# Performance work log

Hardware: AMD Instinct MI355X
Metric: run time of the kernel (lower is better)

## Reference

```python
import jax, jax.numpy as jnp
import numpy as np

MODEL = 1024
HEADS = 16
HEAD_DIM = MODEL // HEADS
INNER = 4096
EPS = 1e-5


def _layer_norm(x, gamma, beta):
    mu = jnp.mean(x, axis=-1, keepdims=True)
    var = jnp.mean((x - mu) ** 2, axis=-1, keepdims=True)
    return (x - mu) * jax.lax.rsqrt(var + EPS) * gamma + beta


def setup_inputs() -> dict:
    key = jax.random.key(0)
    ks = jax.random.split(key, 12)
    B, S = 4, 2048
    s_in = 1.0 / np.sqrt(MODEL)
    s_ff = 1.0 / np.sqrt(INNER)
    return {
        "x": jax.random.normal(ks[0], (B, S, MODEL), jnp.float32),
        "mask": jnp.ones((B, 1, 1, S), jnp.int32),
        "Wq": jax.random.normal(ks[1], (MODEL, MODEL), jnp.float32) * s_in,
        "bq": jnp.zeros((MODEL,), jnp.float32),
        "Wk": jax.random.normal(ks[2], (MODEL, MODEL), jnp.float32) * s_in,
        "bk": jnp.zeros((MODEL,), jnp.float32),
        "Wv": jax.random.normal(ks[3], (MODEL, MODEL), jnp.float32) * s_in,
        "bv": jnp.zeros((MODEL,), jnp.float32),
        "Wo": jax.random.normal(ks[4], (MODEL, MODEL), jnp.float32) * s_in,
        "bo": jnp.zeros((MODEL,), jnp.float32),
        "g1": jnp.ones((MODEL,), jnp.float32),
        "beta1": jnp.zeros((MODEL,), jnp.float32),
        "W1": jax.random.normal(ks[5], (MODEL, INNER), jnp.float32) * s_in,
        "b1": jnp.zeros((INNER,), jnp.float32),
        "W2": jax.random.normal(ks[6], (INNER, MODEL), jnp.float32) * s_ff,
        "b2": jnp.zeros((MODEL,), jnp.float32),
        "g2": jnp.ones((MODEL,), jnp.float32),
        "beta2": jnp.zeros((MODEL,), jnp.float32),
    }


def reference(x, mask, Wq, bq, Wk, bk, Wv, bv, Wo, bo, g1, beta1, W1, b1, W2, b2, g2, beta2):
    B, S, _ = x.shape
    temp = jnp.sqrt(jnp.float32(HEAD_DIM))
    # projections -> [B, H, S, Dh]
    q = (x @ Wq + bq).reshape(B, S, HEADS, HEAD_DIM).transpose(0, 2, 1, 3)
    k = (x @ Wk + bk).reshape(B, S, HEADS, HEAD_DIM).transpose(0, 2, 1, 3)
    v = (x @ Wv + bv).reshape(B, S, HEADS, HEAD_DIM).transpose(0, 2, 1, 3)
    # scores [B, H, S, S]
    scores = jnp.einsum("bhqd,bhkd->bhqk", q / temp, k)
    scores = jnp.where(mask == 0, jnp.float32(-1e10), scores)
    attn = jax.nn.softmax(scores, axis=-1)
    ctx = jnp.einsum("bhqk,bhkd->bhqd", attn, v)
    ctx = ctx.transpose(0, 2, 1, 3).reshape(B, S, MODEL)
    attn_out = ctx @ Wo + bo
    x = _layer_norm(x + attn_out, g1, beta1)
    ff = jax.nn.relu(x @ W1 + b1) @ W2 + b2
    x = _layer_norm(x + ff, g2, beta2)
    return x
```

## Files before the change

### kernel.cpp

```cpp
#include <hip/hip_runtime.h>
#include <stdint.h>

#define MODEL 1024
#define INNER 4096
#define NHEADS 16
#define HDIM 64
#define BATCH 4
#define SEQ 2048
#define MROWS (BATCH*SEQ)

#define QSCALE 0.18033688011112042f
#define DEFER_THR 11.541560327111708f

typedef __bf16 bf16x8 __attribute__((ext_vector_type(8)));
typedef float f32x4 __attribute__((ext_vector_type(4)));
typedef unsigned short ushort4v __attribute__((ext_vector_type(4)));

extern "C" __device__ float __ocml_native_exp2_f32(float);

__device__ __forceinline__ unsigned short f2bf(float f) {
  unsigned u = __builtin_bit_cast(unsigned, f);
  u += 0x7FFFu + ((u >> 16) & 1u);
  return (unsigned short)(u >> 16);
}
__device__ __forceinline__ unsigned packbf_trunc(float lo, float hi) {
  return (__builtin_bit_cast(unsigned, hi) & 0xFFFF0000u) |
         (__builtin_bit_cast(unsigned, lo) >> 16);
}

#define AS1 __attribute__((address_space(1)))
#define AS3 __attribute__((address_space(3)))
__device__ __forceinline__ void gload_lds16(const void* g, void* l) {
  __builtin_amdgcn_global_load_lds((const AS1 void*)g, (AS3 void*)l, 16, 0, 0);
}

__global__ __launch_bounds__(256) void k_cvt(const float* __restrict__ in,
                                             unsigned short* __restrict__ out, int n4) {
  int i = blockIdx.x * 256 + threadIdx.x;
  if (i < n4) {
    float4 v = ((const float4*)in)[i];
    ushort4v o = { f2bf(v.x), f2bf(v.y), f2bf(v.z), f2bf(v.w) };
    ((ushort4v*)out)[i] = o;
  }
}

__global__ __launch_bounds__(256) void k_bcat(const float* __restrict__ bq,
                                              const float* __restrict__ bk,
                                              const float* __restrict__ bv,
                                              float* __restrict__ o) {
  int i = blockIdx.x * 256 + threadIdx.x;
  o[i] = (i < 1024) ? bq[i] : (i < 2048) ? bk[i - 1024] : bv[i - 2048];
}

__global__ __launch_bounds__(256) void k_transpose(const float* __restrict__ W,
                                                   unsigned short* __restrict__ Wt,
                                                   int K, int N) {
  __shared__ float tile[32][33];
  const int n0 = blockIdx.x * 32, k0 = blockIdx.y * 32;
  const int c = threadIdx.x & 31, r4 = threadIdx.x >> 5;
#pragma unroll
  for (int i = 0; i < 4; i++) {
    int r = r4 + i * 8;
    tile[r][c] = W[(size_t)(k0 + r) * N + n0 + c];
  }
  __syncthreads();
#pragma unroll
  for (int i = 0; i < 4; i++) {
    int r = r4 + i * 8;
    Wt[(size_t)(n0 + r) * K + k0 + c] = f2bf(tile[c][r]);
  }
}

template <int MODE, bool SPLIT>
__global__ __launch_bounds__(512, 2) void k_gemm(const unsigned short* __restrict__ A,
                                                 const unsigned short* __restrict__ Bt,
                                                 const float* __restrict__ bias,
                                                 void* __restrict__ out0,
                                                 void* __restrict__ out1,
                                                 void* __restrict__ out2,
                                                 int M, int N, int Kfull) {
  __shared__ unsigned short As[3 * 256 * 32];
  __shared__ unsigned short Bs[3 * 256 * 32];
  const int t = threadIdx.x;
  const int lane = t & 63;
  const int w = t >> 6;
  const int li = lane & 15, lg = lane >> 4;
  const int wm8 = w >> 2, wn4 = w & 3;

  const unsigned nwg = gridDim.x * gridDim.y;
  const unsigned lin = blockIdx.y * gridDim.x + blockIdx.x;
  const unsigned q8 = nwg >> 3, r8 = nwg & 7, xcd = lin & 7, pos = lin >> 3;
  const unsigned swz = (xcd < r8 ? xcd * (q8 + 1) : r8 * (q8 + 1) + (xcd - r8) * q8) + pos;
  int bx = swz % gridDim.x, by = swz / gridDim.x;

  int kp = 0, Ksub = Kfull;
  if (SPLIT) {
    const int hx = gridDim.x >> 1;
    kp = bx >= hx;
    bx -= kp * hx;
    Ksub = Kfull >> 1;
  }
  const int bm = by * 256, bn = bx * 256;
  const size_t koff = (size_t)kp * Ksub;
  const int NT = Ksub / 32;

  const int sr0 = w * 16 + (lane >> 2);
  const int sr1 = sr0 + 128;
  const int sl = lane & 3;
  const unsigned short* pA0 = A + (size_t)(bm + sr0) * Kfull + koff + ((sl ^ ((sr0 >> 1) & 3)) << 3);
  const unsigned short* pA1 = A + (size_t)(bm + sr1) * Kfull + koff + ((sl ^ ((sr1 >> 1) & 3)) << 3);
  const unsigned short* pB0 = Bt + (size_t)(bn + sr0) * Kfull + koff + ((sl ^ ((sr0 >> 1) & 3)) << 3);
  const unsigned short* pB1 = Bt + (size_t)(bn + sr1) * Kfull + koff + ((sl ^ ((sr1 >> 1) & 3)) << 3);

  f32x4 acc[8][4] = {};

  auto stageA = [&](int buf, int tt) {
    gload_lds16(pA0 + tt * 32, &As[buf * 8192 + w * 512]);
    gload_lds16(pA1 + tt * 32, &As[buf * 8192 + 4096 + w * 512]);
  };
  auto stageB = [&](int buf, int tt) {
    gload_lds16(pB0 + tt * 32, &Bs[buf * 8192 + w * 512]);
    gload_lds16(pB1 + tt * 32, &Bs[buf * 8192 + 4096 + w * 512]);
  };

  stageA(0, 0); stageB(0, 0);
  stageA(1, 1); stageB(1, 1);
  asm volatile("s_waitcnt vmcnt(4)" ::: "memory");
  __builtin_amdgcn_s_barrier();

  int buf = 0;
  for (int tt = 0; tt < NT; ++tt) {
    const int nb = (buf + 2 >= 3) ? buf - 1 : buf + 2;
    const unsigned short* Ab = &As[buf * 8192];
    const unsigned short* Bb = &Bs[buf * 8192];
    bf16x8 av[4], bv_[4];
#pragma unroll
    for (int m = 0; m < 4; m++) {
      const int r = wm8 * 128 + m * 16 + li;
      av[m] = *(const bf16x8*)&Ab[r * 32 + ((lg ^ ((r >> 1) & 3)) << 3)];
    }
#pragma unroll
    for (int n = 0; n < 4; n++) {
      const int r = wn4 * 64 + n * 16 + li;
      bv_[n] = *(const bf16x8*)&Bb[r * 32 + ((lg ^ ((r >> 1) & 3)) << 3)];
    }
    if (tt + 2 < NT) stageA(nb, tt + 2);
    __builtin_amdgcn_s_barrier();
    __builtin_amdgcn_s_setprio(1);
#pragma unroll
    for (int m = 0; m < 4; m++)
#pragma unroll
      for (int n = 0; n < 4; n++)
        acc[m][n] = __builtin_amdgcn_mfma_f32_16x16x32_bf16(av[m], bv_[n], acc[m][n], 0, 0, 0);
    __builtin_amdgcn_s_setprio(0);
    bf16x8 av2[4];
#pragma unroll
    for (int m = 0; m < 4; m++) {
      const int r = wm8 * 128 + 64 + m * 16 + li;
      av2[m] = *(const bf16x8*)&Ab[r * 32 + ((lg ^ ((r >> 1) & 3)) << 3)];
    }
    if (tt + 2 < NT) stageB(nb, tt + 2);
    __builtin_amdgcn_s_barrier();
    __builtin_amdgcn_s_setprio(1);
#pragma unroll
    for (int m = 0; m < 4; m++)
#pragma unroll
      for (int n = 0; n < 4; n++)
        acc[m + 4][n] = __builtin_amdgcn_mfma_f32_16x16x32_bf16(av2[m], bv_[n], acc[m + 4][n], 0, 0, 0);
    __builtin_amdgcn_s_setprio(0);
    if (tt + 2 < NT) asm volatile("s_waitcnt vmcnt(4)" ::: "memory");
    else             asm volatile("s_waitcnt vmcnt(0)" ::: "memory");
    __builtin_amdgcn_s_barrier();
    buf = (buf == 2) ? 0 : buf + 1;
  }

#pragma unroll
  for (int m = 0; m < 8; m++) {
    const int row0 = bm + wm8 * 128 + m * 16 + lg * 4;
#pragma unroll
    for (int n = 0; n < 4; n++) {
      const int gcol = bn + wn4 * 64 + n * 16 + li;
      if (MODE == 0) {
        float* dst = (float*)(kp ? out1 : out0);
        const float bvc = (!SPLIT || kp == 0) ? bias[gcol] : 0.f;
#pragma unroll
        for (int j = 0; j < 4; j++)
          dst[(size_t)(row0 + j) * N + gcol] = acc[m][n][j] + bvc;
      } else if (MODE == 2) {
        const float bvc = bias[gcol];
#pragma unroll
        for (int j = 0; j < 4; j++)
          ((unsigned short*)out0)[(size_t)(row0 + j) * N + gcol] = f2bf(fmaxf(acc[m][n][j] + bvc, 0.f));
      } else {
        const float bvc = bias[gcol];
        const int region = gcol >> 10, lcol = gcol & 1023;
        if (region < 2) {
          unsigned short* dst = (unsigned short*)(region ? out1 : out0);
          const float sc = region ? 1.f : QSCALE;
#pragma unroll
          for (int j = 0; j < 4; j++)
            dst[(size_t)(row0 + j) * MODEL + lcol] = f2bf((acc[m][n][j] + bvc) * sc);
        } else {
          ushort4v o = {f2bf(acc[m][n][0] + bvc), f2bf(acc[m][n][1] + bvc),
                        f2bf(acc[m][n][2] + bvc), f2bf(acc[m][n][3] + bvc)};
          *(ushort4v*)&((unsigned short*)out2)[(size_t)lcol * MROWS + row0] = o;
        }
      }
    }
  }
}

__global__ __launch_bounds__(256, 3) void k_attn(const unsigned short* __restrict__ q,
                                                 const unsigned short* __restrict__ kptr,
                                                 const unsigned short* __restrict__ vt,
                                                 const int* __restrict__ mask,
                                                 unsigned short* __restrict__ ctx) {
  __shared__ unsigned short Ks[2][64 * 64];
  __shared__ unsigned short Vs[2][64 * 64];
  __shared__ unsigned short Ps[4][32 * 64];
  const int t = threadIdx.x, lane = t & 63, w = t >> 6;
  const int li = lane & 15, lg = lane >> 4;
  const int bh = blockIdx.y, b = bh >> 4, h = bh & 15;
  const int q0 = blockIdx.x * 128;
  const size_t basebs = (size_t)b * SEQ;
  const int sw = 8 * (li & 7);
  const int srow = lane >> 3;
  const int scsw = ((lane & 7) ^ srow) * 8;

  auto stageKV = [&](int buf, int kt) {
#pragma unroll
    for (int i = 0; i < 2; i++) {
      const int row = i * 32 + w * 8 + srow;
      gload_lds16(kptr + (basebs + kt + row) * MODEL + h * 64 + scsw,
                  &Ks[buf][i * 2048 + w * 512]);
    }
#pragma unroll
    for (int i = 0; i < 2; i++) {
      const int row = i * 32 + w * 8 + srow;
      gload_lds16(vt + (size_t)(h * 64 + row) * MROWS + basebs + kt + scsw,
                  &Vs[buf][i * 2048 + w * 512]);
    }
  };

  stageKV(0, 0);

  bf16x8 qf[2][2];
#pragma unroll
  for (int m = 0; m < 2; m++)
#pragma unroll
    for (int kk = 0; kk < 2; kk++) {
      int row = q0 + w * 32 + m * 16 + li;
      qf[m][kk] = *(const bf16x8*)&q[(basebs + row) * MODEL + h * 64 + kk * 32 + lg * 8];
    }

  const unsigned short one_bits = 0x3F80;
  const __bf16 oneb = __builtin_bit_cast(__bf16, one_bits);
  const bf16x8 ones = {oneb, oneb, oneb, oneb, oneb, oneb, oneb, oneb};

  f32x4 acc_oT[4][2] = {};
  f32x4 acc_l[2] = {};
  float mrow[2] = {-3e38f, -3e38f};

  int cur = 0;
  for (int kt = 0; kt < SEQ; kt += 64) {
    int4 mk4[4];
#pragma unroll
    for (int n = 0; n < 4; n++)
      mk4[n] = *(const int4*)&mask[b * SEQ + kt + n * 16 + lg * 4];

    const bool notlast = (kt + 64 < SEQ);
    if (notlast) {
      stageKV(cur ^ 1, kt + 64);
      asm volatile("s_waitcnt vmcnt(8)" ::: "memory");
    } else {
      asm volatile("s_waitcnt vmcnt(4)" ::: "memory");
    }
    __builtin_amdgcn_s_barrier();

    f32x4 sacc[2][4] = {};
    __builtin_amdgcn_s_setprio(1);
#pragma unroll
    for (int n = 0; n < 4; n++) {
      const int rb = (n * 16 + li) * 64;
      bf16x8 kf0 = *(const bf16x8*)&Ks[cur][rb + ((lg * 8) ^ sw)];
      bf16x8 kf1 = *(const bf16x8*)&Ks[cur][rb + ((32 + lg * 8) ^ sw)];
#pragma unroll
      for (int m = 0; m < 2; m++) {
        sacc[m][n] = __builtin_amdgcn_mfma_f32_16x16x32_bf16(kf0, qf[m][0], sacc[m][n], 0, 0, 0);
        sacc[m][n] = __builtin_amdgcn_mfma_f32_16x16x32_bf16(kf1, qf[m][1], sacc[m][n], 0, 0, 0);
      }
    }
    __builtin_amdgcn_s_setprio(0);

    int mand = mk4[0].x & mk4[0].y & mk4[0].z & mk4[0].w;
    mand &= mk4[1].x & mk4[1].y & mk4[1].z & mk4[1].w;
    mand &= mk4[2].x & mk4[2].y & mk4[2].z & mk4[2].w;
    mand &= mk4[3].x & mk4[3].y & mk4[3].z & mk4[3].w;
    const bool fast = __all(mand != 0);

#pragma unroll
    for (int m = 0; m < 2; m++) {
      if (!fast) {
#pragma unroll
        for (int n = 0; n < 4; n++) {
          const int mks[4] = {mk4[n].x, mk4[n].y, mk4[n].z, mk4[n].w};
#pragma unroll
          for (int j = 0; j < 4; j++)
            sacc[m][n][j] = (mks[j] == 0) ? -1e30f : sacc[m][n][j];
        }
      }
      float t0 = fmaxf(fmaxf(sacc[m][0][0], sacc[m][0][1]), fmaxf(sacc[m][0][2], sacc[m][0][3]));
      float t1 = fmaxf(fmaxf(sacc[m][1][0], sacc[m][1][1]), fmaxf(sacc[m][1][2], sacc[m][1][3]));
      float t2 = fmaxf(fmaxf(sacc[m][2][0], sacc[m][2][1]), fmaxf(sacc[m][2][2], sacc[m][2][3]));
      float t3 = fmaxf(fmaxf(sacc[m][3][0], sacc[m][3][1]), fmaxf(sacc[m][3][2], sacc[m][3][3]));
      float rmax = fmaxf(fmaxf(t0, t1), fmaxf(t2, t3));
      rmax = fmaxf(rmax, __shfl_xor(rmax, 16));
      rmax = fmaxf(rmax, __shfl_xor(rmax, 32));
      if (!__all(rmax <= mrow[m] + DEFER_THR)) {
        float mnew = fmaxf(mrow[m], rmax);
        float alpha = __ocml_native_exp2_f32(mrow[m] - mnew);
        mrow[m] = mnew;
        acc_l[m] *= alpha;
#pragma unroll
        for (int nd = 0; nd < 4; nd++)
#pragma unroll
          for (int j = 0; j < 4; j++) acc_oT[nd][m][j] *= alpha;
      }
#pragma unroll
      for (int n = 0; n < 4; n++) {
        float p0 = __ocml_native_exp2_f32(sacc[m][n][0] - mrow[m]);
        float p1 = __ocml_native_exp2_f32(sacc[m][n][1] - mrow[m]);
        float p2 = __ocml_native_exp2_f32(sacc[m][n][2] - mrow[m]);
        float p3 = __ocml_native_exp2_f32(sacc[m][n][3] - mrow[m]);
        uint2 pk = {packbf_trunc(p0, p1), packbf_trunc(p2, p3)};
        *(uint2*)&Ps[w][(m * 16 + li) * 64 + ((n * 16 + lg * 4) ^ sw)] = pk;
      }
    }
    asm volatile("s_waitcnt lgkmcnt(0)" ::: "memory");

    __builtin_amdgcn_s_setprio(1);
#pragma unroll
    for (int n2 = 0; n2 < 2; n2++) {
      const int kof = (n2 * 32 + lg * 8) ^ sw;
      bf16x8 pa0 = *(const bf16x8*)&Ps[w][li * 64 + kof];
      bf16x8 pa1 = *(const bf16x8*)&Ps[w][(16 + li) * 64 + kof];
#pragma unroll
      for (int nd = 0; nd < 4; nd++) {
        bf16x8 vfr = *(const bf16x8*)&Vs[cur][(nd * 16 + li) * 64 + kof];
        acc_oT[nd][0] = __builtin_amdgcn_mfma_f32_16x16x32_bf16(vfr, pa0, acc_oT[nd][0], 0, 0, 0);
        acc_oT[nd][1] = __builtin_amdgcn_mfma_f32_16x16x32_bf16(vfr, pa1, acc_oT[nd][1], 0, 0, 0);
      }
      acc_l[0] = __builtin_amdgcn_mfma_f32_16x16x32_bf16(ones, pa0, acc_l[0], 0, 0, 0);
      acc_l[1] = __builtin_amdgcn_mfma_f32_16x16x32_bf16(ones, pa1, acc_l[1], 0, 0, 0);
    }
    __builtin_amdgcn_s_setprio(0);
    __builtin_amdgcn_sched_barrier(0);
    __builtin_amdgcn_s_barrier();
    cur ^= 1;
  }

#pragma unroll
  for (int m = 0; m < 2; m++) {
    const float rl = 1.f / acc_l[m][0];
    const size_t rowoff = (basebs + q0 + w * 32 + m * 16 + li) * (size_t)MODEL + h * 64;
#pragma unroll
    for (int nd = 0; nd < 4; nd++) {
      ushort4v o = {f2bf(acc_oT[nd][m][0] * rl), f2bf(acc_oT[nd][m][1] * rl),
                    f2bf(acc_oT[nd][m][2] * rl), f2bf(acc_oT[nd][m][3] * rl)};
      *(ushort4v*)&ctx[rowoff + nd * 16 + lg * 4] = o;
    }
  }
}

template <bool WB>
__global__ __launch_bounds__(256) void k_ln3(const float* __restrict__ a,
                                             const float* __restrict__ b0,
                                             const float* __restrict__ b1,
                                             const float* __restrict__ gamma,
                                             const float* __restrict__ beta,
                                             float* __restrict__ outf,
                                             unsigned short* __restrict__ outb) {
  const int row = blockIdx.x;
  const int t = threadIdx.x;
  const size_t off = (size_t)row * MODEL + t * 4;
  float4 xa = *(const float4*)&a[off];
  float4 x0 = *(const float4*)&b0[off];
  float4 x1 = *(const float4*)&b1[off];
  float z0 = xa.x + x0.x + x1.x, z1 = xa.y + x0.y + x1.y;
  float z2 = xa.z + x0.z + x1.z, z3 = xa.w + x0.w + x1.w;
  float s = z0 + z1 + z2 + z3;
  float ss = z0 * z0 + z1 * z1 + z2 * z2 + z3 * z3;
#pragma unroll
  for (int o = 1; o < 64; o <<= 1) { s += __shfl_xor(s, o); ss += __shfl_xor(ss, o); }
  __shared__ float red[8];
  const int lane = t & 63, w = t >> 6;
  if (lane == 0) { red[w] = s; red[4 + w] = ss; }
  __syncthreads();
  s = red[0] + red[1] + red[2] + red[3];
  ss = red[4] + red[5] + red[6] + red[7];
  float mu = s * (1.f / MODEL);
  float var = ss * (1.f / MODEL) - mu * mu;
  float inv = rsqrtf(var + 1e-5f);
  float4 g = *(const float4*)&gamma[t * 4];
  float4 be = *(const float4*)&beta[t * 4];
  float o0 = (z0 - mu) * inv * g.x + be.x;
  float o1 = (z1 - mu) * inv * g.y + be.y;
  float o2 = (z2 - mu) * inv * g.z + be.z;
  float o3 = (z3 - mu) * inv * g.w + be.w;
  float4 ov = {o0, o1, o2, o3};
  *(float4*)&outf[off] = ov;
  if (WB) {
    ushort4v ob = {f2bf(o0), f2bf(o1), f2bf(o2), f2bf(o3)};
    *(ushort4v*)&outb[off] = ob;
  }
}

extern "C" void kernel_launch(void* const* d_in, const int* in_sizes, int n_in,
                              void* d_out, int out_size, void* d_ws, size_t ws_size,
                              hipStream_t stream) {
  (void)in_sizes; (void)n_in; (void)out_size; (void)ws_size;
  const float* x   = (const float*)d_in[0];
  const int*   mask= (const int*)d_in[1];
  const float* Wq  = (const float*)d_in[2];
  const float* bq  = (const float*)d_in[3];
  const float* Wk  = (const float*)d_in[4];
  const float* bk  = (const float*)d_in[5];
  const float* Wv  = (const float*)d_in[6];
  const float* bv  = (const float*)d_in[7];
  const float* Wo  = (const float*)d_in[8];
  const float* bo  = (const float*)d_in[9];
  const float* g1  = (const float*)d_in[10];
  const float* be1 = (const float*)d_in[11];
  const float* W1  = (const float*)d_in[12];
  const float* b1  = (const float*)d_in[13];
  const float* W2  = (const float*)d_in[14];
  const float* b2  = (const float*)d_in[15];
  const float* g2  = (const float*)d_in[16];
  const float* be2 = (const float*)d_in[17];
  float* out = (float*)d_out;

  char* p = (char*)d_ws;
  auto alloc = [&](size_t bytes) { char* r = p; p += (bytes + 255) & ~(size_t)255; return r; };
  unsigned short* xb    = (unsigned short*)alloc((size_t)MROWS * MODEL * 2);
  unsigned short* y1b   = (unsigned short*)alloc((size_t)MROWS * MODEL * 2);
  unsigned short* WqkvT = (unsigned short*)alloc((size_t)3 * MODEL * MODEL * 2);
  unsigned short* WoT   = (unsigned short*)alloc((size_t)MODEL * MODEL * 2);
  unsigned short* W1T   = (unsigned short*)alloc((size_t)MODEL * INNER * 2);
  unsigned short* W2T   = (unsigned short*)alloc((size_t)INNER * MODEL * 2);
  float* bqkv           = (float*)alloc(3072 * 4);
  unsigned short* qb    = (unsigned short*)alloc((size_t)MROWS * MODEL * 2);
  unsigned short* kb    = (unsigned short*)alloc((size_t)MROWS * MODEL * 2);
  unsigned short* vtb   = (unsigned short*)alloc((size_t)MODEL * MROWS * 2);
  unsigned short* ctxb  = (unsigned short*)alloc((size_t)MROWS * MODEL * 2);
  float* attn_out       = (float*)alloc((size_t)MROWS * MODEL * 4);
  float* y1f            = (float*)alloc((size_t)MROWS * MODEL * 4);
  unsigned short* h1 = qb;
  float* p1wo = (float*)kb;
  float* ff   = attn_out;
  float* p1ff = (float*)xb;

  k_cvt<<<(MROWS * MODEL / 4) / 256, 256, 0, stream>>>(x, xb, MROWS * MODEL / 4);
  k_bcat<<<12, 256, 0, stream>>>(bq, bk, bv, bqkv);
  k_transpose<<<dim3(MODEL / 32, MODEL / 32), 256, 0, stream>>>(Wq, WqkvT, MODEL, MODEL);
  k_transpose<<<dim3(MODEL / 32, MODEL / 32), 256, 0, stream>>>(Wk, WqkvT + (size_t)MODEL * MODEL, MODEL, MODEL);
  k_transpose<<<dim3(MODEL / 32, MODEL / 32), 256, 0, stream>>>(Wv, WqkvT + (size_t)2 * MODEL * MODEL, MODEL, MODEL);
  k_transpose<<<dim3(MODEL / 32, MODEL / 32), 256, 0, stream>>>(Wo, WoT, MODEL, MODEL);
  k_transpose<<<dim3(INNER / 32, MODEL / 32), 256, 0, stream>>>(W1, W1T, MODEL, INNER);
  k_transpose<<<dim3(MODEL / 32, INNER / 32), 256, 0, stream>>>(W2, W2T, INNER, MODEL);

  k_gemm<3, false><<<dim3(12, MROWS / 256), 512, 0, stream>>>(xb, WqkvT, bqkv, qb, kb, vtb, MROWS, 3072, MODEL);

  k_attn<<<dim3(SEQ / 128, BATCH * NHEADS), 256, 0, stream>>>(qb, kb, vtb, mask, ctxb);

  k_gemm<0, true><<<dim3(8, MROWS / 256), 512, 0, stream>>>(ctxb, WoT, bo, attn_out, p1wo, nullptr, MROWS, MODEL, MODEL);

  k_ln3<true><<<MROWS, 256, 0, stream>>>(x, attn_out, p1wo, g1, be1, y1f, y1b);

  k_gemm<2, false><<<dim3(INNER / 256, MROWS / 256), 512, 0, stream>>>(y1b, W1T, b1, h1, nullptr, nullptr, MROWS, INNER, MODEL);

  k_gemm<0, true><<<dim3(8, MROWS / 256), 512, 0, stream>>>(h1, W2T, b2, ff, p1ff, nullptr, MROWS, MODEL, INNER);

  k_ln3<false><<<MROWS, 256, 0, stream>>>(y1f, ff, p1ff, g2, be2, out, nullptr);
}
```

Before: 457.2 us.

## Rewrite attention with 32x32 MFMA register-resident P and bf16 intermediates

The attention kernel switches from 16x16x32 to 32x32x16 MFMA tiles. P now stays in registers, exchanged with cross-lane shuffles instead of an LDS round trip. The row sum is computed with shuffles instead of a ones-matrix MFMA, and the mask is precomputed into a shared bitmask; occupancy is raised to 4 blocks. Separately, the split-K GEMM partials and the LayerNorm inputs and residual are stored as bf16 instead of fp32, which cuts memory traffic but adds rounding error, including in the second residual path.

```diff
diff --git a/kernel.cpp b/kernel.cpp
--- a/kernel.cpp
+++ b/kernel.cpp
@@ -14,7 +14,9 @@
 
 typedef __bf16 bf16x8 __attribute__((ext_vector_type(8)));
 typedef float f32x4 __attribute__((ext_vector_type(4)));
+typedef float f32x16 __attribute__((ext_vector_type(16)));
 typedef unsigned short ushort4v __attribute__((ext_vector_type(4)));
+typedef unsigned uint4v __attribute__((ext_vector_type(4)));
 
 extern "C" __device__ float __ocml_native_exp2_f32(float);
 
@@ -22,6 +24,9 @@
   unsigned u = __builtin_bit_cast(unsigned, f);
   u += 0x7FFFu + ((u >> 16) & 1u);
   return (unsigned short)(u >> 16);
+}
+__device__ __forceinline__ float bf2f(unsigned short u) {
+  return __builtin_bit_cast(float, (unsigned)u << 16);
 }
 __device__ __forceinline__ unsigned packbf_trunc(float lo, float hi) {
   return (__builtin_bit_cast(unsigned, hi) & 0xFFFF0000u) |
@@ -181,11 +186,11 @@
     for (int n = 0; n < 4; n++) {
       const int gcol = bn + wn4 * 64 + n * 16 + li;
       if (MODE == 0) {
-        float* dst = (float*)(kp ? out1 : out0);
-        const float bvc = (!SPLIT || kp == 0) ? bias[gcol] : 0.f;
+        unsigned short* dst = (unsigned short*)(kp ? out1 : out0);
+        const float bvc = (kp == 0) ? bias[gcol] : 0.f;
 #pragma unroll
         for (int j = 0; j < 4; j++)
-          dst[(size_t)(row0 + j) * N + gcol] = acc[m][n][j] + bvc;
+          dst[(size_t)(row0 + j) * N + gcol] = f2bf(acc[m][n][j] + bvc);
       } else if (MODE == 2) {
         const float bvc = bias[gcol];
 #pragma unroll
@@ -210,22 +215,33 @@
   }
 }
 
-__global__ __launch_bounds__(256, 3) void k_attn(const unsigned short* __restrict__ q,
+__global__ __launch_bounds__(256, 4) void k_attn(const unsigned short* __restrict__ q,
                                                  const unsigned short* __restrict__ kptr,
                                                  const unsigned short* __restrict__ vt,
                                                  const int* __restrict__ mask,
                                                  unsigned short* __restrict__ ctx) {
   __shared__ unsigned short Ks[2][64 * 64];
   __shared__ unsigned short Vs[2][64 * 64];
-  __shared__ unsigned short Ps[4][32 * 64];
+  __shared__ unsigned maskw[SEQ / 32];
   const int t = threadIdx.x, lane = t & 63, w = t >> 6;
-  const int li = lane & 15, lg = lane >> 4;
+  const int l31 = lane & 31, hi = lane >> 5;
   const int bh = blockIdx.y, b = bh >> 4, h = bh & 15;
   const int q0 = blockIdx.x * 128;
   const size_t basebs = (size_t)b * SEQ;
-  const int sw = 8 * (li & 7);
   const int srow = lane >> 3;
   const int scsw = ((lane & 7) ^ srow) * 8;
+
+  {
+    const int base = b * SEQ + t * 8;
+    int4 m0 = *(const int4*)&mask[base];
+    int4 m1 = *(const int4*)&mask[base + 4];
+    unsigned byte = (unsigned)(m0.x != 0) | ((unsigned)(m0.y != 0) << 1) |
+                    ((unsigned)(m0.z != 0) << 2) | ((unsigned)(m0.w != 0) << 3) |
+                    ((unsigned)(m1.x != 0) << 4) | ((unsigned)(m1.y != 0) << 5) |
+                    ((unsigned)(m1.z != 0) << 6) | ((unsigned)(m1.w != 0) << 7);
+    ((unsigned char*)maskw)[t] = (unsigned char)byte;
+  }
+  __syncthreads();
 
   auto stageKV = [&](int buf, int kt) {
 #pragma unroll
@@ -244,114 +260,109 @@
 
   stageKV(0, 0);
 
-  bf16x8 qf[2][2];
-#pragma unroll
-  for (int m = 0; m < 2; m++)
-#pragma unroll
-    for (int kk = 0; kk < 2; kk++) {
-      int row = q0 + w * 32 + m * 16 + li;
-      qf[m][kk] = *(const bf16x8*)&q[(basebs + row) * MODEL + h * 64 + kk * 32 + lg * 8];
-    }
-
-  const unsigned short one_bits = 0x3F80;
-  const __bf16 oneb = __builtin_bit_cast(__bf16, one_bits);
-  const bf16x8 ones = {oneb, oneb, oneb, oneb, oneb, oneb, oneb, oneb};
-
-  f32x4 acc_oT[4][2] = {};
-  f32x4 acc_l[2] = {};
-  float mrow[2] = {-3e38f, -3e38f};
+  bf16x8 qf[4];
+#pragma unroll
+  for (int s = 0; s < 4; s++)
+    qf[s] = *(const bf16x8*)&q[(basebs + q0 + w * 32 + l31) * MODEL + h * 64 + s * 16 + hi * 8];
+
+  f32x16 acc_o[2] = {};
+  float mrow = -3e38f, lrow = 0.f;
 
   int cur = 0;
   for (int kt = 0; kt < SEQ; kt += 64) {
-    int4 mk4[4];
-#pragma unroll
-    for (int n = 0; n < 4; n++)
-      mk4[n] = *(const int4*)&mask[b * SEQ + kt + n * 16 + lg * 4];
-
-    const bool notlast = (kt + 64 < SEQ);
-    if (notlast) {
+    if (kt + 64 < SEQ) {
       stageKV(cur ^ 1, kt + 64);
-      asm volatile("s_waitcnt vmcnt(8)" ::: "memory");
+      asm volatile("s_waitcnt vmcnt(4)" ::: "memory");
     } else {
-      asm volatile("s_waitcnt vmcnt(4)" ::: "memory");
+      asm volatile("s_waitcnt vmcnt(0)" ::: "memory");
     }
     __builtin_amdgcn_s_barrier();
 
-    f32x4 sacc[2][4] = {};
+    f32x16 sacc[2] = {};
     __builtin_amdgcn_s_setprio(1);
 #pragma unroll
-    for (int n = 0; n < 4; n++) {
-      const int rb = (n * 16 + li) * 64;
-      bf16x8 kf0 = *(const bf16x8*)&Ks[cur][rb + ((lg * 8) ^ sw)];
-      bf16x8 kf1 = *(const bf16x8*)&Ks[cur][rb + ((32 + lg * 8) ^ sw)];
-#pragma unroll
-      for (int m = 0; m < 2; m++) {
-        sacc[m][n] = __builtin_amdgcn_mfma_f32_16x16x32_bf16(kf0, qf[m][0], sacc[m][n], 0, 0, 0);
-        sacc[m][n] = __builtin_amdgcn_mfma_f32_16x16x32_bf16(kf1, qf[m][1], sacc[m][n], 0, 0, 0);
+    for (int kb = 0; kb < 2; kb++) {
+#pragma unroll
+      for (int s = 0; s < 4; s++) {
+        bf16x8 kf = *(const bf16x8*)&Ks[cur][(kb * 32 + l31) * 64 + (((s * 2 + hi) ^ (l31 & 7)) << 3)];
+        sacc[kb] = __builtin_amdgcn_mfma_f32_32x32x16_bf16(kf, qf[s], sacc[kb], 0, 0, 0);
       }
     }
     __builtin_amdgcn_s_setprio(0);
 
-    int mand = mk4[0].x & mk4[0].y & mk4[0].z & mk4[0].w;
-    mand &= mk4[1].x & mk4[1].y & mk4[1].z & mk4[1].w;
-    mand &= mk4[2].x & mk4[2].y & mk4[2].z & mk4[2].w;
-    mand &= mk4[3].x & mk4[3].y & mk4[3].z & mk4[3].w;
-    const bool fast = __all(mand != 0);
-
-#pragma unroll
-    for (int m = 0; m < 2; m++) {
-      if (!fast) {
-#pragma unroll
-        for (int n = 0; n < 4; n++) {
-          const int mks[4] = {mk4[n].x, mk4[n].y, mk4[n].z, mk4[n].w};
-#pragma unroll
-          for (int j = 0; j < 4; j++)
-            sacc[m][n][j] = (mks[j] == 0) ? -1e30f : sacc[m][n][j];
+    const unsigned W0 = maskw[(kt >> 5)], W1 = maskw[(kt >> 5) + 1];
+    if ((W0 & W1) != 0xFFFFFFFFu) {
+#pragma unroll
+      for (int kb = 0; kb < 2; kb++) {
+        const unsigned Wb = kb ? W1 : W0;
+#pragma unroll
+        for (int rq = 0; rq < 4; rq++)
+#pragma unroll
+          for (int e = 0; e < 4; e++) {
+            const int r = rq * 4 + e;
+            sacc[kb][r] = ((Wb >> (e + 8 * rq + 4 * hi)) & 1u) ? sacc[kb][r] : -1e30f;
+          }
+      }
+    }
+
+    float rmax = -3e38f;
+#pragma unroll
+    for (int kb = 0; kb < 2; kb++) {
+      float t0 = fmaxf(fmaxf(sacc[kb][0], sacc[kb][1]), fmaxf(sacc[kb][2], sacc[kb][3]));
+      float t1 = fmaxf(fmaxf(sacc[kb][4], sacc[kb][5]), fmaxf(sacc[kb][6], sacc[kb][7]));
+      float t2 = fmaxf(fmaxf(sacc[kb][8], sacc[kb][9]), fmaxf(sacc[kb][10], sacc[kb][11]));
+      float t3 = fmaxf(fmaxf(sacc[kb][12], sacc[kb][13]), fmaxf(sacc[kb][14], sacc[kb][15]));
+      rmax = fmaxf(rmax, fmaxf(fmaxf(t0, t1), fmaxf(t2, t3)));
+    }
+    rmax = fmaxf(rmax, __shfl_xor(rmax, 32));
+
+    if (!__all(rmax <= mrow + DEFER_THR)) {
+      float mnew = fmaxf(mrow, rmax);
+      float alpha = __ocml_native_exp2_f32(mrow - mnew);
+      mrow = mnew;
+      lrow *= alpha;
+#pragma unroll
+      for (int db = 0; db < 2; db++)
+#pragma unroll
+        for (int r = 0; r < 16; r++) acc_o[db][r] *= alpha;
+    }
+
+    unsigned pk[2][8];
+    float tsum = 0.f;
+#pragma unroll
+    for (int kb = 0; kb < 2; kb++)
+#pragma unroll
+      for (int i = 0; i < 8; i++) {
+        float p0 = __ocml_native_exp2_f32(sacc[kb][2 * i] - mrow);
+        float p1 = __ocml_native_exp2_f32(sacc[kb][2 * i + 1] - mrow);
+        tsum += p0 + p1;
+        pk[kb][i] = packbf_trunc(p0, p1);
+      }
+    lrow += tsum + __shfl_xor(tsum, 32);
+
+    __builtin_amdgcn_s_setprio(1);
+#pragma unroll
+    for (int kb = 0; kb < 2; kb++) {
+#pragma unroll
+      for (int s = 0; s < 2; s++) {
+        const unsigned own0 = pk[kb][4 * s + 0], own1 = pk[kb][4 * s + 1];
+        const unsigned own2 = pk[kb][4 * s + 2], own3 = pk[kb][4 * s + 3];
+        const unsigned par0 = (unsigned)__shfl_xor((int)own0, 32);
+        const unsigned par1 = (unsigned)__shfl_xor((int)own1, 32);
+        const unsigned par2 = (unsigned)__shfl_xor((int)own2, 32);
+        const unsigned par3 = (unsigned)__shfl_xor((int)own3, 32);
+        const unsigned pu0 = hi ? par2 : own0;
+        const unsigned pu1 = hi ? par3 : own1;
+        const unsigned pu2 = hi ? own2 : par0;
+        const unsigned pu3 = hi ? own3 : par1;
+        uint4v pu = {pu0, pu1, pu2, pu3};
+        bf16x8 paf = __builtin_bit_cast(bf16x8, pu);
+#pragma unroll
+        for (int db = 0; db < 2; db++) {
+          bf16x8 vf = *(const bf16x8*)&Vs[cur][(db * 32 + l31) * 64 + (((kb * 4 + s * 2 + hi) ^ (l31 & 7)) << 3)];
+          acc_o[db] = __builtin_amdgcn_mfma_f32_32x32x16_bf16(vf, paf, acc_o[db], 0, 0, 0);
         }
       }
-      float t0 = fmaxf(fmaxf(sacc[m][0][0], sacc[m][0][1]), fmaxf(sacc[m][0][2], sacc[m][0][3]));
-      float t1 = fmaxf(fmaxf(sacc[m][1][0], sacc[m][1][1]), fmaxf(sacc[m][1][2], sacc[m][1][3]));
-      float t2 = fmaxf(fmaxf(sacc[m][2][0], sacc[m][2][1]), fmaxf(sacc[m][2][2], sacc[m][2][3]));
-      float t3 = fmaxf(fmaxf(sacc[m][3][0], sacc[m][3][1]), fmaxf(sacc[m][3][2], sacc[m][3][3]));
-      float rmax = fmaxf(fmaxf(t0, t1), fmaxf(t2, t3));
-      rmax = fmaxf(rmax, __shfl_xor(rmax, 16));
-      rmax = fmaxf(rmax, __shfl_xor(rmax, 32));
-      if (!__all(rmax <= mrow[m] + DEFER_THR)) {
-        float mnew = fmaxf(mrow[m], rmax);
-        float alpha = __ocml_native_exp2_f32(mrow[m] - mnew);
-        mrow[m] = mnew;
-        acc_l[m] *= alpha;
-#pragma unroll
-        for (int nd = 0; nd < 4; nd++)
-#pragma unroll
-          for (int j = 0; j < 4; j++) acc_oT[nd][m][j] *= alpha;
-      }
-#pragma unroll
-      for (int n = 0; n < 4; n++) {
-        float p0 = __ocml_native_exp2_f32(sacc[m][n][0] - mrow[m]);
-        float p1 = __ocml_native_exp2_f32(sacc[m][n][1] - mrow[m]);
-        float p2 = __ocml_native_exp2_f32(sacc[m][n][2] - mrow[m]);
-        float p3 = __ocml_native_exp2_f32(sacc[m][n][3] - mrow[m]);
-        uint2 pk = {packbf_trunc(p0, p1), packbf_trunc(p2, p3)};
-        *(uint2*)&Ps[w][(m * 16 + li) * 64 + ((n * 16 + lg * 4) ^ sw)] = pk;
-      }
-    }
-    asm volatile("s_waitcnt lgkmcnt(0)" ::: "memory");
-
-    __builtin_amdgcn_s_setprio(1);
-#pragma unroll
-    for (int n2 = 0; n2 < 2; n2++) {
-      const int kof = (n2 * 32 + lg * 8) ^ sw;
-      bf16x8 pa0 = *(const bf16x8*)&Ps[w][li * 64 + kof];
-      bf16x8 pa1 = *(const bf16x8*)&Ps[w][(16 + li) * 64 + kof];
-#pragma unroll
-      for (int nd = 0; nd < 4; nd++) {
-        bf16x8 vfr = *(const bf16x8*)&Vs[cur][(nd * 16 + li) * 64 + kof];
-        acc_oT[nd][0] = __builtin_amdgcn_mfma_f32_16x16x32_bf16(vfr, pa0, acc_oT[nd][0], 0, 0, 0);
-        acc_oT[nd][1] = __builtin_amdgcn_mfma_f32_16x16x32_bf16(vfr, pa1, acc_oT[nd][1], 0, 0, 0);
-      }
-      acc_l[0] = __builtin_amdgcn_mfma_f32_16x16x32_bf16(ones, pa0, acc_l[0], 0, 0, 0);
-      acc_l[1] = __builtin_amdgcn_mfma_f32_16x16x32_bf16(ones, pa1, acc_l[1], 0, 0, 0);
     }
     __builtin_amdgcn_s_setprio(0);
     __builtin_amdgcn_sched_barrier(0);
@@ -359,35 +370,43 @@
     cur ^= 1;
   }
 
-#pragma unroll
-  for (int m = 0; m < 2; m++) {
-    const float rl = 1.f / acc_l[m][0];
-    const size_t rowoff = (basebs + q0 + w * 32 + m * 16 + li) * (size_t)MODEL + h * 64;
-#pragma unroll
-    for (int nd = 0; nd < 4; nd++) {
-      ushort4v o = {f2bf(acc_oT[nd][m][0] * rl), f2bf(acc_oT[nd][m][1] * rl),
-                    f2bf(acc_oT[nd][m][2] * rl), f2bf(acc_oT[nd][m][3] * rl)};
-      *(ushort4v*)&ctx[rowoff + nd * 16 + lg * 4] = o;
-    }
-  }
-}
-
-template <bool WB>
-__global__ __launch_bounds__(256) void k_ln3(const float* __restrict__ a,
-                                             const float* __restrict__ b0,
-                                             const float* __restrict__ b1,
-                                             const float* __restrict__ gamma,
-                                             const float* __restrict__ beta,
-                                             float* __restrict__ outf,
-                                             unsigned short* __restrict__ outb) {
+  const float rl = 1.f / lrow;
+  const size_t rowoff = (basebs + q0 + w * 32 + l31) * (size_t)MODEL + h * 64;
+#pragma unroll
+  for (int db = 0; db < 2; db++)
+#pragma unroll
+    for (int rq = 0; rq < 4; rq++) {
+      const int r = rq * 4;
+      ushort4v o = {f2bf(acc_o[db][r] * rl), f2bf(acc_o[db][r + 1] * rl),
+                    f2bf(acc_o[db][r + 2] * rl), f2bf(acc_o[db][r + 3] * rl)};
+      *(ushort4v*)&ctx[rowoff + db * 32 + rq * 8 + 4 * hi] = o;
+    }
+}
+
+template <bool AF32>
+__global__ __launch_bounds__(256) void k_ln(const void* __restrict__ a,
+                                            const unsigned short* __restrict__ b0,
+                                            const unsigned short* __restrict__ b1,
+                                            const float* __restrict__ gamma,
+                                            const float* __restrict__ beta,
+                                            float* __restrict__ outf,
+                                            unsigned short* __restrict__ outb) {
   const int row = blockIdx.x;
   const int t = threadIdx.x;
   const size_t off = (size_t)row * MODEL + t * 4;
-  float4 xa = *(const float4*)&a[off];
-  float4 x0 = *(const float4*)&b0[off];
-  float4 x1 = *(const float4*)&b1[off];
-  float z0 = xa.x + x0.x + x1.x, z1 = xa.y + x0.y + x1.y;
-  float z2 = xa.z + x0.z + x1.z, z3 = xa.w + x0.w + x1.w;
+  float4 xa;
+  if (AF32) {
+    xa = *(const float4*)((const float*)a + off);
+  } else {
+    ushort4v av = *(const ushort4v*)((const unsigned short*)a + off);
+    xa = {bf2f(av.x), bf2f(av.y), bf2f(av.z), bf2f(av.w)};
+  }
+  ushort4v u0 = *(const ushort4v*)&b0[off];
+  ushort4v u1 = *(const ushort4v*)&b1[off];
+  float z0 = xa.x + bf2f(u0.x) + bf2f(u1.x);
+  float z1 = xa.y + bf2f(u0.y) + bf2f(u1.y);
+  float z2 = xa.z + bf2f(u0.z) + bf2f(u1.z);
+  float z3 = xa.w + bf2f(u0.w) + bf2f(u1.w);
   float s = z0 + z1 + z2 + z3;
   float ss = z0 * z0 + z1 * z1 + z2 * z2 + z3 * z3;
 #pragma unroll
@@ -407,11 +426,12 @@
   float o1 = (z1 - mu) * inv * g.y + be.y;
   float o2 = (z2 - mu) * inv * g.z + be.z;
   float o3 = (z3 - mu) * inv * g.w + be.w;
-  float4 ov = {o0, o1, o2, o3};
-  *(float4*)&outf[off] = ov;
-  if (WB) {
+  if (AF32) {
     ushort4v ob = {f2bf(o0), f2bf(o1), f2bf(o2), f2bf(o3)};
     *(ushort4v*)&outb[off] = ob;
+  } else {
+    float4 ov = {o0, o1, o2, o3};
+    *(float4*)&outf[off] = ov;
   }
 }
 
@@ -452,12 +472,11 @@
   unsigned short* kb    = (unsigned short*)alloc((size_t)MROWS * MODEL * 2);
   unsigned short* vtb   = (unsigned short*)alloc((size_t)MODEL * MROWS * 2);
   unsigned short* ctxb  = (unsigned short*)alloc((size_t)MROWS * MODEL * 2);
-  float* attn_out       = (float*)alloc((size_t)MROWS * MODEL * 4);
-  float* y1f            = (float*)alloc((size_t)MROWS * MODEL * 4);
-  unsigned short* h1 = qb;
-  float* p1wo = (float*)kb;
-  float* ff   = attn_out;
-  float* p1ff = (float*)xb;
+  unsigned short* ao0   = (unsigned short*)alloc((size_t)MROWS * MODEL * 2);
+  unsigned short* ao1   = (unsigned short*)alloc((size_t)MROWS * MODEL * 2);
+  unsigned short* h1  = qb;
+  unsigned short* ff0 = ao0;
+  unsigned short* ff1 = ao1;
 
   k_cvt<<<(MROWS * MODEL / 4) / 256, 256, 0, stream>>>(x, xb, MROWS * MODEL / 4);
   k_bcat<<<12, 256, 0, stream>>>(bq, bk, bv, bqkv);
@@ -472,13 +491,13 @@
 
   k_attn<<<dim3(SEQ / 128, BATCH * NHEADS), 256, 0, stream>>>(qb, kb, vtb, mask, ctxb);
 
-  k_gemm<0, true><<<dim3(8, MROWS / 256), 512, 0, stream>>>(ctxb, WoT, bo, attn_out, p1wo, nullptr, MROWS, MODEL, MODEL);
-
-  k_ln3<true><<<MROWS, 256, 0, stream>>>(x, attn_out, p1wo, g1, be1, y1f, y1b);
+  k_gemm<0, true><<<dim3(8, MROWS / 256), 512, 0, stream>>>(ctxb, WoT, bo, ao0, ao1, nullptr, MROWS, MODEL, MODEL);
+
+  k_ln<true><<<MROWS, 256, 0, stream>>>(x, ao0, ao1, g1, be1, nullptr, y1b);
 
   k_gemm<2, false><<<dim3(INNER / 256, MROWS / 256), 512, 0, stream>>>(y1b, W1T, b1, h1, nullptr, nullptr, MROWS, INNER, MODEL);
 
-  k_gemm<0, true><<<dim3(8, MROWS / 256), 512, 0, stream>>>(h1, W2T, b2, ff, p1ff, nullptr, MROWS, MODEL, INNER);
-
-  k_ln3<false><<<MROWS, 256, 0, stream>>>(y1f, ff, p1ff, g2, be2, out, nullptr);
-}
+  k_gemm<0, true><<<dim3(8, MROWS / 256), 512, 0, stream>>>(h1, W2T, b2, ff0, ff1, nullptr, MROWS, MODEL, INNER);
+
+  k_ln<false><<<MROWS, 256, 0, stream>>>(y1b, ff0, ff1, g2, be2, out, nullptr);
+}
```

Result: faster. 421.3 us (-7.8%).
